# Kernel tuning notes

Hardware: AMD Instinct MI355X
Metric: run time of the kernel (lower is better)

The kernel has to match this reference:

```python
import jax, jax.numpy as jnp
import numpy as np

RADIUS = 0.2
NUM_POINTS = 32
MAX_POINTS = 60
BN_EPS = 1e-5


def _bn(x, g, b, m, v):
    # BatchNorm in eval mode (running stats), channels-last broadcast
    return g * (x - m) * jax.lax.rsqrt(v + BN_EPS) + b


def setup_inputs() -> dict:
    key = jax.random.key(0)
    nk = lambda i: jax.random.fold_in(key, i)
    B, NQ, NC, HC = 2, 4096, 8192, 64
    inp = {}
    inp['p_query'] = jax.random.uniform(nk(0), (B, NQ, 3), dtype=jnp.float32)
    inp['p_context'] = jax.random.uniform(nk(1), (B, NC, 3), dtype=jnp.float32)
    inp['h_context'] = jax.random.normal(nk(2), (B, NC, HC), dtype=jnp.float32)

    def lin(i, o, ci):
        return (jax.random.normal(nk(i), (o, ci), jnp.float32) / np.sqrt(ci).astype(np.float32),
                0.01 * jax.random.normal(nk(i + 1), (o,), jnp.float32))

    def bnp(i, c):
        return (1.0 + 0.1 * jax.random.normal(nk(i), (c,), jnp.float32),
                0.1 * jax.random.normal(nk(i + 1), (c,), jnp.float32),
                0.1 * jax.random.normal(nk(i + 2), (c,), jnp.float32),
                0.5 + jax.random.uniform(nk(i + 3), (c,), jnp.float32))

    inp['w_xyz'], inp['b_xyz'] = lin(10, 64, 3)
    # pointwise 1x1 Conv2d MLP: 128 -> 128 -> 128 -> 256 (BN after each conv)
    inp['pw_w1'], inp['pw_b1'] = lin(12, 128, 128)
    inp['pw_g1'], inp['pw_be1'], inp['pw_m1'], inp['pw_v1'] = bnp(14, 128)
    inp['pw_w2'], inp['pw_b2'] = lin(20, 128, 128)
    inp['pw_g2'], inp['pw_be2'], inp['pw_m2'], inp['pw_v2'] = bnp(22, 128)
    inp['pw_w3'], inp['pw_b3'] = lin(28, 256, 128)
    inp['pw_g3'], inp['pw_be3'], inp['pw_m3'], inp['pw_v3'] = bnp(30, 256)
    # global 1x1 Conv1d MLP: 256 -> 128 -> 64 -> 3 (BN+ReLU between, none on last)
    inp['g_w1'], inp['g_b1'] = lin(36, 128, 256)
    inp['g_g1'], inp['g_be1'], inp['g_m1'], inp['g_v1'] = bnp(38, 128)
    inp['g_w2'], inp['g_b2'] = lin(44, 64, 128)
    inp['g_g2'], inp['g_be2'], inp['g_m2'], inp['g_v2'] = bnp(46, 64)
    inp['g_w3'], inp['g_b3'] = lin(52, 3, 64)
    return inp


def reference(p_query, p_context, h_context, w_xyz, b_xyz,
              pw_w1, pw_b1, pw_g1, pw_be1, pw_m1, pw_v1,
              pw_w2, pw_b2, pw_g2, pw_be2, pw_m2, pw_v2,
              pw_w3, pw_b3, pw_g3, pw_be3, pw_m3, pw_v3,
              g_w1, g_b1, g_g1, g_be1, g_m1, g_v1,
              g_w2, g_b2, g_g2, g_be2, g_m2, g_v2,
              g_w3, g_b3):
    N = p_context.shape[1]
    # knn_points: squared distances, K smallest sorted ascending
    d = (jnp.sum(p_query ** 2, -1)[:, :, None]
         - 2.0 * jnp.einsum('bqd,bnd->bqn', p_query, p_context)
         + jnp.sum(p_context ** 2, -1)[:, None, :])  # [B,NQ,NC]
    neg, idx = jax.lax.top_k(-d, MAX_POINTS)
    dist = -neg  # [B,NQ,K] ascending
    knn_idx = jnp.where(dist > RADIUS ** 2, N + 1, idx)
    idx = knn_idx[:, :, :NUM_POINTS]
    dist = dist[:, :, :NUM_POINTS]
    mask = idx == N + 1
    idx = jnp.where(mask, 0, idx)
    dist = jnp.where(mask, 0.0, dist)
    gather = jax.vmap(lambda a, i: a[i])
    pts = gather(p_context, idx)        # [B,NQ,P,3]
    h_group = gather(h_context, idx)    # [B,NQ,P,HC]
    p_rel = pts - p_query[:, :, None, :]
    h_rel = p_rel @ w_xyz.T + b_xyz     # Linear(3 -> 64)
    h = jnp.concatenate([h_rel, h_group], -1)  # [B,NQ,P,128]
    h = jax.nn.relu(_bn(h @ pw_w1.T + pw_b1, pw_g1, pw_be1, pw_m1, pw_v1))
    h = jax.nn.relu(_bn(h @ pw_w2.T + pw_b2, pw_g2, pw_be2, pw_m2, pw_v2))
    h = _bn(h @ pw_w3.T + pw_b3, pw_g3, pw_be3, pw_m3, pw_v3)  # [B,NQ,P,256]
    # cosine radius weighting (note: dist is SQUARED distance, faithful to source)
    c = 0.5 * (jnp.cos(dist * (np.pi / RADIUS)) + 1.0)
    c = jnp.where((dist <= RADIUS) & (dist > 0.0), c, 0.0)
    y = jnp.sum(h * c[..., None], axis=2)  # masked weighted pool over neighbors -> [B,NQ,256]
    y = jax.nn.relu(_bn(y @ g_w1.T + g_b1, g_g1, g_be1, g_m1, g_v1))
    y = jax.nn.relu(_bn(y @ g_w2.T + g_b2, g_g2, g_be2, g_m2, g_v2))
    return y @ g_w3.T + g_b3  # [B,NQ,3]
```

## Files before the change

kernel.cpp:

```cpp
#include <hip/hip_runtime.h>
#include <hip/hip_bf16.h>
#include <math.h>

#define BB 2
#define NQ 4096
#define NC 8192
#define KNN 32
#define WCAP 512
#define QB 4
#define MROWS 128
#define BN_EPS 1e-5f

typedef __attribute__((ext_vector_type(8))) short s16x8;
typedef __attribute__((ext_vector_type(4))) float f32x4;

#define WS_IDX   0
#define WS_CW    1048576
#define WS_Z     2097152
#define WS_SQ    6291456
#define WS_PCF   6324224
#define WS_PIDX  6586368
#define WS_CELL  6651904
#define WS_CCNT  6717440
#define WS_COFS  6718464
#define WS_W1    6719488
#define WS_W2    6752256
#define WS_W3    6785024
#define WS_GW1   6850560
#define WS_GW2   6916096
#define WS_F3    6932480
#define WS_FG1   6934528
#define WS_FG2   6935552

__device__ inline int swz(int row, int kbyte, int rb) {
    return row * rb + (kbyte ^ ((row & 7) << 4));
}
__device__ inline unsigned short f2bf(float x) {
    __hip_bfloat16 h = __float2bfloat16(x);
    return *reinterpret_cast<unsigned short*>(&h);
}
__device__ inline float bf2f(unsigned short u) {
    return __uint_as_float(((unsigned)u) << 16);
}
__device__ inline int cell1d(float x) {
    int c = (int)floorf(x * 5.0f);
    return c < 0 ? 0 : (c > 4 ? 4 : c);
}

__device__ inline void mk_img(const float* __restrict__ src, int R, int K, char* dst, int t, int NT)
{
    int rbg = (K * 2) / 16;
    int ng = R * rbg;
    for (int g = t; g < ng; g += NT) {
        int row = g / rbg;
        int b16 = (g - row * rbg) * 16;
        int sb  = b16 ^ ((row & 7) << 4);
        const float* s = src + row * K + sb / 2;
        union { s16x8 v; unsigned short u[8]; } pk;
#pragma unroll
        for (int j = 0; j < 8; ++j) pk.u[j] = f2bf(s[j]);
        *(s16x8*)(dst + row * (K * 2) + b16) = pk.v;
    }
}

__global__ __launch_bounds__(256) void prep_kernel(
    const float* __restrict__ pc,
    const float* __restrict__ w1, const float* __restrict__ w2, const float* __restrict__ w3,
    const float* __restrict__ gw1, const float* __restrict__ gw2,
    const float* __restrict__ g3, const float* __restrict__ b3, const float* __restrict__ m3,
    const float* __restrict__ v3, const float* __restrict__ be3,
    const float* __restrict__ gg1, const float* __restrict__ gb1, const float* __restrict__ gm1,
    const float* __restrict__ gv1, const float* __restrict__ gbe1,
    const float* __restrict__ gg2, const float* __restrict__ gb2, const float* __restrict__ gm2,
    const float* __restrict__ gv2, const float* __restrict__ gbe2,
    char* __restrict__ ws)
{
    const int t = blockIdx.x * 256 + threadIdx.x;
    const int NT = gridDim.x * 256;

    int* cell = (int*)(ws + WS_CELL);
    int* ccnt = (int*)(ws + WS_CCNT);
    for (int i = t; i < BB * NC; i += NT) {
        float x = pc[i*3+0], y = pc[i*3+1], z = pc[i*3+2];
        int c = (cell1d(z)*5 + cell1d(y))*5 + cell1d(x);
        cell[i] = c;
        atomicAdd(&ccnt[(i >> 13)*128 + c], 1);
    }

    mk_img(w1,  128, 128, ws + WS_W1,  t, NT);
    mk_img(w2,  128, 128, ws + WS_W2,  t, NT);
    mk_img(w3,  256, 128, ws + WS_W3,  t, NT);
    mk_img(gw1, 128, 256, ws + WS_GW1, t, NT);
    mk_img(gw2,  64, 128, ws + WS_GW2, t, NT);

    if (t < 256) {
        float s = g3[t] * rsqrtf(v3[t] + BN_EPS);
        ((float2*)(ws + WS_F3))[t] = make_float2(s, s * (b3[t] - m3[t]) + be3[t]);
    }
    if (t < 128) {
        float s = gg1[t] * rsqrtf(gv1[t] + BN_EPS);
        ((float2*)(ws + WS_FG1))[t] = make_float2(s, s * (gb1[t] - gm1[t]) + gbe1[t]);
    }
    if (t < 64) {
        float s = gg2[t] * rsqrtf(gv2[t] + BN_EPS);
        ((float2*)(ws + WS_FG2))[t] = make_float2(s, s * (gb2[t] - gm2[t]) + gbe2[t]);
    }
}

__global__ __launch_bounds__(128) void scan_kernel(char* __restrict__ ws)
{
    int* ccnt = (int*)(ws + WS_CCNT);
    int* cofs = (int*)(ws + WS_COFS);
    const int wv = threadIdx.x >> 6, lane = threadIdx.x & 63;
    const int base = wv * 128;
    int a = (lane < 125) ? ccnt[base + lane] : 0;
    int b = (64 + lane < 125) ? ccnt[base + 64 + lane] : 0;
    int ai = a, bi = b;
    for (int d = 1; d < 64; d <<= 1) {
        int t = __shfl_up(ai, d, 64);
        if (lane >= d) ai += t;
    }
    int totA = __shfl(ai, 63, 64);
    for (int d = 1; d < 64; d <<= 1) {
        int t = __shfl_up(bi, d, 64);
        if (lane >= d) bi += t;
    }
    int exA = ai - a;
    int exB = totA + bi - b;
    cofs[base + lane] = exA;       cofs[base + 64 + lane] = exB;
    ccnt[base + lane] = exA;       ccnt[base + 64 + lane] = exB;
}

__global__ __launch_bounds__(256) void scatter_kernel(
    const float* __restrict__ pc, char* __restrict__ ws)
{
    const int i = blockIdx.x * 256 + threadIdx.x;
    if (i >= BB * NC) return;
    const int b = i >> 13, loc = i & (NC - 1);
    int* cell = (int*)(ws + WS_CELL);
    int* cur  = (int*)(ws + WS_CCNT);
    float4* pcf = (float4*)(ws + WS_PCF);
    int*    pidx = (int*)(ws + WS_PIDX);
    int c = cell[i];
    int pos = atomicAdd(&cur[b*128 + c], 1);
    float x = pc[i*3+0], y = pc[i*3+1], z = pc[i*3+2];
    float w = (x*x + y*y) + z*z;
    pcf[(size_t)b*NC + pos]  = make_float4(x, y, z, w);
    pidx[(size_t)b*NC + pos] = loc;
}

__device__ inline void cmpxu(unsigned long long& k, int j, bool up) {
    unsigned long long ok = __shfl_xor(k, j, 64);
    bool lower = ((threadIdx.x & 63) & j) == 0;
    bool take = (lower == up) ? (k > ok) : (k < ok);
    if (take) k = ok;
}
__device__ inline void sortasc64(unsigned long long& k) {
    const int lane = threadIdx.x & 63;
    for (int kk = 2; kk <= 64; kk <<= 1)
        for (int j = kk >> 1; j > 0; j >>= 1)
            cmpxu(k, j, (lane & kk) == 0);
}
__device__ inline void sortdesc64(unsigned long long& k) {
    const int lane = threadIdx.x & 63;
    for (int kk = 2; kk <= 64; kk <<= 1)
        for (int j = kk >> 1; j > 0; j >>= 1)
            cmpxu(k, j, (lane & kk) != 0);
}
__device__ inline void merge128(unsigned long long& k0, unsigned long long& k1) {
    if (k0 > k1) { unsigned long long t = k0; k0 = k1; k1 = t; }
#pragma unroll
    for (int j = 32; j > 0; j >>= 1) { cmpxu(k0, j, true); cmpxu(k1, j, true); }
}
__device__ inline void cmpx64(unsigned long long& k, int& p, int j, bool up) {
    unsigned long long ok = __shfl_xor(k, j, 64);
    int op = __shfl_xor(p, j, 64);
    bool lower = ((threadIdx.x & 63) & j) == 0;
    bool gt = (k > ok) || (k == ok && p > op);
    bool take = (lower == up) ? gt : !gt;
    if (take) { k = ok; p = op; }
}
__device__ inline void sortasc64kp(unsigned long long& k, int& p) {
    const int lane = threadIdx.x & 63;
    for (int kk = 2; kk <= 64; kk <<= 1)
        for (int j = kk >> 1; j > 0; j >>= 1)
            cmpx64(k, p, j, (lane & kk) == 0);
}

__global__ __launch_bounds__(256) void knn_kernel(
    const float* __restrict__ pq, const float* __restrict__ pc,
    const float4* __restrict__ pcf, const int* __restrict__ pidx,
    const int* __restrict__ cofs,
    int* __restrict__ idx_out, float* __restrict__ cw_out)
{
    __shared__ unsigned long long kbuf[4][WCAP];

    const int tid = threadIdx.x, lane = tid & 63, w = tid >> 6;
    const int gq = blockIdx.x * 4 + w;
    const int b = gq >> 12;

    const float qxf = pq[gq*3+0], qyf = pq[gq*3+1], qzf = pq[gq*3+2];
    const double qx = (double)qxf, qy = (double)qyf, qz = (double)qzf;
    const double sq = qx*qx + qy*qy + qz*qz;
    const float  sqf = (float)sq;
    const double R2d = 0.2 * 0.2;
    const float  R2f = 0.04f + 1e-4f;

    const float4* pcfb = pcf + (size_t)b * NC;
    const int*    pidb = pidx + (size_t)b * NC;
    const int*    cb   = cofs + b * 128;
    const float*  pcb  = pc + (size_t)b * NC * 3;

    int xlo = (int)floorf((qxf - 0.2f) * 5.0f - 1e-3f); xlo = xlo < 0 ? 0 : xlo;
    int xhi = (int)floorf((qxf + 0.2f) * 5.0f + 1e-3f); xhi = xhi > 4 ? 4 : xhi;
    int ylo = (int)floorf((qyf - 0.2f) * 5.0f - 1e-3f); ylo = ylo < 0 ? 0 : ylo;
    int yhi = (int)floorf((qyf + 0.2f) * 5.0f + 1e-3f); yhi = yhi > 4 ? 4 : yhi;
    int zlo = (int)floorf((qzf - 0.2f) * 5.0f - 1e-3f); zlo = zlo < 0 ? 0 : zlo;
    int zhi = (int)floorf((qzf + 0.2f) * 5.0f + 1e-3f); zhi = zhi > 4 ? 4 : zhi;

    const unsigned long long lt = (lane == 63) ? ~0ULL >> 1 : (1ULL << lane) - 1;
    int cnt = 0;
    for (int zi = zlo; zi <= zhi; ++zi) {
        for (int yi = ylo; yi <= yhi; ++yi) {
            int row = (zi*5 + yi)*5;
            int s = cb[row + xlo], e = cb[row + xhi + 1];
            for (int t0 = s; t0 < e; t0 += 64) {
                int t = t0 + lane;
                bool pred = false;
                unsigned long long key = ~0ULL;
                if (t < e) {
                    float4 cd = pcfb[t];
                    float dot = (qxf*cd.x + qyf*cd.y) + qzf*cd.z;
                    float d   = (sqf - 2.0f*dot) + cd.w;
                    pred = (d <= R2f);
                    if (pred) {
                        float dc = fmaxf(d, 0.0f);
                        key = ((unsigned long long)__float_as_uint(dc) << 32)
                            | (unsigned)pidb[t];
                    }
                }
                unsigned long long mask = __ballot(pred);
                if (pred) {
                    int pos = cnt + __popcll(mask & lt);
                    if (pos < WCAP) kbuf[w][pos] = key;
                }
                cnt += __popcll(mask);
            }
        }
    }
    if (cnt > WCAP) cnt = WCAP;

    unsigned long long k0 = (lane < cnt)      ? kbuf[w][lane]      : ~0ULL;
    unsigned long long k1 = (64 + lane < cnt) ? kbuf[w][64 + lane] : ~0ULL;
    sortasc64(k0);
    sortdesc64(k1);
    merge128(k0, k1);
    int consumed = 128;
    while (consumed < cnt) {
        int i1 = consumed + lane;
        k1 = (i1 < cnt) ? kbuf[w][i1] : ~0ULL;
        sortdesc64(k1);
        merge128(k0, k1);
        consumed += 64;
    }

    unsigned long long kf = ~0ULL;
    int pf = 0x7fffffff;
    if (k0 != ~0ULL) {
        int n = (int)(k0 & 0xffffffffULL);
        double cx = (double)pcb[n*3+0];
        double cy = (double)pcb[n*3+1];
        double cz = (double)pcb[n*3+2];
        double dot = qx*cx + qy*cy + qz*cz;
        double sc  = cx*cx + cy*cy + cz*cz;
        double d   = (sq - 2.0*dot) + sc;
        if (d <= R2d) {
            double dc = d < 0.0 ? 0.0 : d;
            kf = (unsigned long long)__double_as_longlong(dc);
            pf = n;
        }
    }
    sortasc64kp(kf, pf);

    if (lane < KNN) {
        int id = 0; float c = 0.0f;
        if (kf != ~0ULL) {
            id = pf;
            double d = __longlong_as_double((long long)kf);
            if (d > 0.0 && d <= 0.2) {
                double cw = 0.5 * (cos(d * 15.707963267948966) + 1.0);
                c = (float)cw;
            }
        }
        idx_out[gq*KNN + lane] = id;
        cw_out[gq*KNN + lane]  = c;
    }
}

__global__ __launch_bounds__(512, 4) void front_kernel(
    const float* __restrict__ pq, const float* __restrict__ pc, const float* __restrict__ hc,
    const float* __restrict__ w_xyz, const float* __restrict__ b_xyz,
    const float* __restrict__ b1, const float* __restrict__ g1,
    const float* __restrict__ be1, const float* __restrict__ m1, const float* __restrict__ v1,
    const float* __restrict__ b2, const float* __restrict__ g2,
    const float* __restrict__ be2, const float* __restrict__ m2, const float* __restrict__ v2,
    const char* __restrict__ w1img, const char* __restrict__ w2img,
    const int* __restrict__ idx_in, const float* __restrict__ cw_in,
    float* __restrict__ z_buf, float* __restrict__ sq_buf)
{
    __shared__ __align__(16) char smem[74240];
    char*  Ab   = smem;
    char*  Wb   = smem + 32768;
    float* Prel = (float*)(smem + 65536);
    float* Cw   = (float*)(smem + 67072);
    int*   Sidx = (int*)  (smem + 67584);
    float* Sfd  = (float*)(smem + 68096);
    float* Zp   = (float*)(smem + 70144);

    const int tid = threadIdx.x;
    const int qbase = blockIdx.x * QB;
    const int b = qbase >> 12;
    const float* pcb = pc + (size_t)b * NC * 3;
    const float* hcb = hc + (size_t)b * NC * 64;

    if (tid < MROWS) {
        int id = idx_in[qbase*KNN + tid];
        Sidx[tid] = id;
        Cw[tid]   = cw_in[qbase*KNN + tid];
        int gq = qbase + (tid >> 5);
        Prel[tid*3+0] = pcb[id*3+0] - pq[gq*3+0];
        Prel[tid*3+1] = pcb[id*3+1] - pq[gq*3+1];
        Prel[tid*3+2] = pcb[id*3+2] - pq[gq*3+2];
    }
    __syncthreads();

    for (int p = tid; p < MROWS*16; p += 512) {
        int row = p >> 4, seg = p & 15;
        float vals[8];
        if (seg >= 8) {
            const float* src = hcb + (size_t)Sidx[row]*64 + (seg-8)*8;
            float4 u0 = *(const float4*)src;
            float4 u1 = *(const float4*)(src+4);
            vals[0]=u0.x; vals[1]=u0.y; vals[2]=u0.z; vals[3]=u0.w;
            vals[4]=u1.x; vals[5]=u1.y; vals[6]=u1.z; vals[7]=u1.w;
        } else {
            float px = Prel[row*3+0], py = Prel[row*3+1], pz = Prel[row*3+2];
            int c0 = seg*8;
#pragma unroll
            for (int j = 0; j < 8; ++j) {
                int c = c0 + j;
                vals[j] = px*w_xyz[c*3+0] + py*w_xyz[c*3+1] + pz*w_xyz[c*3+2] + b_xyz[c];
            }
        }
        union { s16x8 v; unsigned short u[8]; } pk;
#pragma unroll
        for (int j = 0; j < 8; ++j) pk.u[j] = f2bf(vals[j]);
        *(s16x8*)(Ab + swz(row, seg*16, 256)) = pk.v;
    }
    if (tid < 128) {
        int j = tid;
        float s0 = g1[j] * rsqrtf(v1[j] + BN_EPS);
        Sfd[0*128 + j] = s0; Sfd[1*128 + j] = s0*(b1[j]-m1[j]) + be1[j];
        float s1 = g2[j] * rsqrtf(v2[j] + BN_EPS);
        Sfd[2*128 + j] = s1; Sfd[3*128 + j] = s1*(b2[j]-m2[j]) + be2[j];
    }
    if (tid < QB) {
        float s = 0.0f;
        for (int i = 0; i < KNN; ++i) s += Cw[tid*KNN + i];
        sq_buf[qbase + tid] = s;
    }

    const int l = tid & 63, w = tid >> 6;
    const int r0 = w * 16, cl = l & 15, q4 = l >> 4;

    {
        const s16x8* wimg = (const s16x8*)w1img;
        s16x8* Wv = (s16x8*)Wb;
        for (int p = tid; p < 2048; p += 512) Wv[p] = wimg[p];
        __syncthreads();

        f32x4 acc[8];
#pragma unroll
        for (int nt = 0; nt < 8; ++nt) acc[nt] = (f32x4){0.f,0.f,0.f,0.f};
#pragma unroll
        for (int kk = 0; kk < 4; ++kk) {
            int kbyte = kk*64 + q4*16;
            s16x8 a0 = *(const s16x8*)(Ab + swz(r0 + cl, kbyte, 256));
#pragma unroll
            for (int nt = 0; nt < 8; ++nt) {
                s16x8 bwv = *(const s16x8*)(Wb + swz(nt*16 + cl, kbyte, 256));
                acc[nt] = __builtin_amdgcn_mfma_f32_16x16x32_bf16(a0, bwv, acc[nt], 0, 0, 0);
            }
        }
#pragma unroll
        for (int nt = 0; nt < 8; ++nt) {
            int j = nt*16 + cl;
            float s = Sfd[0*128 + j], t = Sfd[1*128 + j];
#pragma unroll
            for (int r = 0; r < 4; ++r) {
                int row = r0 + q4*4 + r;
                float x = fmaxf(acc[nt][r]*s + t, 0.0f);
                unsigned int me = f2bf(x);
                unsigned int ot = (unsigned int)__shfl_xor((int)me, 1, 64);
                if ((cl & 1) == 0) {
                    unsigned int pk = me | (ot << 16);
                    *(unsigned int*)(Ab + swz(row, j*2, 256)) = pk;
                }
            }
        }
        __syncthreads();
    }

    {
        const s16x8* wimg = (const s16x8*)w2img;
        s16x8* Wv = (s16x8*)Wb;
        for (int p = tid; p < 2048; p += 512) Wv[p] = wimg[p];
        __syncthreads();

        f32x4 acc[8];
#pragma unroll
        for (int nt = 0; nt < 8; ++nt) acc[nt] = (f32x4){0.f,0.f,0.f,0.f};
#pragma unroll
        for (int kk = 0; kk < 4; ++kk) {
            int kbyte = kk*64 + q4*16;
            s16x8 a0 = *(const s16x8*)(Ab + swz(r0 + cl, kbyte, 256));
#pragma unroll
            for (int nt = 0; nt < 8; ++nt) {
                s16x8 bwv = *(const s16x8*)(Wb + swz(nt*16 + cl, kbyte, 256));
                acc[nt] = __builtin_amdgcn_mfma_f32_16x16x32_bf16(a0, bwv, acc[nt], 0, 0, 0);
            }
        }
        float cwr[4];
#pragma unroll
        for (int r = 0; r < 4; ++r) cwr[r] = Cw[r0 + q4*4 + r];
        float zp[8];
#pragma unroll
        for (int nt = 0; nt < 8; ++nt) {
            int j = nt*16 + cl;
            float s = Sfd[2*128 + j], t = Sfd[3*128 + j];
            float sum = 0.0f;
#pragma unroll
            for (int r = 0; r < 4; ++r) {
                float x = fmaxf(acc[nt][r]*s + t, 0.0f);
                sum += cwr[r] * x;
            }
            sum += __shfl_xor(sum, 16, 64);
            sum += __shfl_xor(sum, 32, 64);
            zp[nt] = sum;
        }
        if (q4 == 0) {
#pragma unroll
            for (int nt = 0; nt < 8; ++nt) Zp[w*128 + nt*16 + cl] = zp[nt];
        }
        __syncthreads();
    }

    {
        int q = tid >> 7, col = tid & 127;
        float z = Zp[(2*q)*128 + col] + Zp[(2*q+1)*128 + col];
        z_buf[(size_t)(qbase + q)*128 + col] = z;
    }
}

__global__ __launch_bounds__(256) void tail_kernel(
    const char* __restrict__ w3img, const char* __restrict__ gw1img, const char* __restrict__ gw2img,
    const float2* __restrict__ f3, const float2* __restrict__ fg1, const float2* __restrict__ fg2,
    const float* __restrict__ z_buf, const float* __restrict__ sq_buf,
    const float* __restrict__ gw3, const float* __restrict__ gb3,
    float* __restrict__ out)
{
    __shared__ __align__(16) char smem[123136];
    char* A1 = smem;
    char* A2 = smem + 16384;
    char* A4 = smem + 49152;
    char* Wb = smem + 57344;
    float* Ssm = (float*)(smem + 122880);

    const int tid = threadIdx.x;
    const int q0 = blockIdx.x * 64;

    for (int g = tid; g < 1024; g += 256) {
        int row = g >> 4, seg = g & 15;
        const float* zs = z_buf + (size_t)(q0 + row)*128 + seg*8;
        float4 u0 = *(const float4*)zs;
        float4 u1 = *(const float4*)(zs+4);
        union { s16x8 v; unsigned short u[8]; } pk;
        pk.u[0]=f2bf(u0.x); pk.u[1]=f2bf(u0.y); pk.u[2]=f2bf(u0.z); pk.u[3]=f2bf(u0.w);
        pk.u[4]=f2bf(u1.x); pk.u[5]=f2bf(u1.y); pk.u[6]=f2bf(u1.z); pk.u[7]=f2bf(u1.w);
        *(s16x8*)(A1 + swz(row, seg*16, 256)) = pk.v;
    }
    for (int p = tid; p < 4096; p += 256) ((s16x8*)Wb)[p] = ((const s16x8*)w3img)[p];
    if (tid < 64) Ssm[tid] = sq_buf[q0 + tid];
    __syncthreads();

    const int l = tid & 63, w = tid >> 6;
    const int r0 = w*16, cl = l & 15, q4 = l >> 4;

    {
        f32x4 acc[16];
#pragma unroll
        for (int nt = 0; nt < 16; ++nt) acc[nt] = (f32x4){0.f,0.f,0.f,0.f};
#pragma unroll
        for (int kk = 0; kk < 4; ++kk) {
            int kbyte = kk*64 + q4*16;
            s16x8 a0 = *(const s16x8*)(A1 + swz(r0 + cl, kbyte, 256));
#pragma unroll
            for (int nt = 0; nt < 16; ++nt) {
                s16x8 bwv = *(const s16x8*)(Wb + swz(nt*16 + cl, kbyte, 256));
                acc[nt] = __builtin_amdgcn_mfma_f32_16x16x32_bf16(a0, bwv, acc[nt], 0, 0, 0);
            }
        }
#pragma unroll
        for (int nt = 0; nt < 16; ++nt) {
            int j = nt*16 + cl;
            float2 f = f3[j];
#pragma unroll
            for (int r = 0; r < 4; ++r) {
                int row = r0 + q4*4 + r;
                float S = Ssm[row];
                float x = f.x*acc[nt][r] + S*f.y;
                *(unsigned short*)(A2 + swz(row, j*2, 512)) = f2bf(x);
            }
        }
    }
    __syncthreads();
    for (int p = tid; p < 4096; p += 256) ((s16x8*)Wb)[p] = ((const s16x8*)gw1img)[p];
    __syncthreads();

    {
        f32x4 acc[8];
#pragma unroll
        for (int nt = 0; nt < 8; ++nt) acc[nt] = (f32x4){0.f,0.f,0.f,0.f};
#pragma unroll
        for (int kk = 0; kk < 8; ++kk) {
            int kbyte = kk*64 + q4*16;
            s16x8 a0 = *(const s16x8*)(A2 + swz(r0 + cl, kbyte, 512));
#pragma unroll
            for (int nt = 0; nt < 8; ++nt) {
                s16x8 bwv = *(const s16x8*)(Wb + swz(nt*16 + cl, kbyte, 512));
                acc[nt] = __builtin_amdgcn_mfma_f32_16x16x32_bf16(a0, bwv, acc[nt], 0, 0, 0);
            }
        }
#pragma unroll
        for (int nt = 0; nt < 8; ++nt) {
            int j = nt*16 + cl;
            float2 f = fg1[j];
#pragma unroll
            for (int r = 0; r < 4; ++r) {
                int row = r0 + q4*4 + r;
                float x = fmaxf(f.x*acc[nt][r] + f.y, 0.0f);
                *(unsigned short*)(A1 + swz(row, j*2, 256)) = f2bf(x);
            }
        }
    }
    __syncthreads();
    for (int p = tid; p < 1024; p += 256) ((s16x8*)Wb)[p] = ((const s16x8*)gw2img)[p];
    __syncthreads();

    {
        f32x4 acc[4];
#pragma unroll
        for (int nt = 0; nt < 4; ++nt) acc[nt] = (f32x4){0.f,0.f,0.f,0.f};
#pragma unroll
        for (int kk = 0; kk < 4; ++kk) {
            int kbyte = kk*64 + q4*16;
            s16x8 a0 = *(const s16x8*)(A1 + swz(r0 + cl, kbyte, 256));
#pragma unroll
            for (int nt = 0; nt < 4; ++nt) {
                s16x8 bwv = *(const s16x8*)(Wb + swz(nt*16 + cl, kbyte, 256));
                acc[nt] = __builtin_amdgcn_mfma_f32_16x16x32_bf16(a0, bwv, acc[nt], 0, 0, 0);
            }
        }
#pragma unroll
        for (int nt = 0; nt < 4; ++nt) {
            int j = nt*16 + cl;
            float2 f = fg2[j];
#pragma unroll
            for (int r = 0; r < 4; ++r) {
                int row = r0 + q4*4 + r;
                float x = fmaxf(f.x*acc[nt][r] + f.y, 0.0f);
                *(unsigned short*)(A4 + swz(row, j*2, 128)) = f2bf(x);
            }
        }
    }
    __syncthreads();

    if (tid < 192) {
        int q = tid / 3, jj = tid - q*3;
        const float* wr = gw3 + jj*64;
        float s = 0.0f;
        for (int k = 0; k < 64; ++k) {
            unsigned short u = *(const unsigned short*)(A4 + swz(q, k*2, 128));
            s += bf2f(u) * wr[k];
        }
        out[(size_t)(q0 + q)*3 + jj] = s + gb3[jj];
    }
}

extern "C" void kernel_launch(void* const* d_in, const int* in_sizes, int n_in,
                              void* d_out, int out_size, void* d_ws, size_t ws_size,
                              hipStream_t stream)
{
    const float* pq    = (const float*)d_in[0];
    const float* pc    = (const float*)d_in[1];
    const float* hc    = (const float*)d_in[2];
    const float* w_xyz = (const float*)d_in[3];
    const float* b_xyz = (const float*)d_in[4];
    const float* w1    = (const float*)d_in[5];
    const float* b1    = (const float*)d_in[6];
    const float* g1    = (const float*)d_in[7];
    const float* be1   = (const float*)d_in[8];
    const float* m1    = (const float*)d_in[9];
    const float* v1    = (const float*)d_in[10];
    const float* w2    = (const float*)d_in[11];
    const float* b2    = (const float*)d_in[12];
    const float* g2    = (const float*)d_in[13];
    const float* be2   = (const float*)d_in[14];
    const float* m2    = (const float*)d_in[15];
    const float* v2    = (const float*)d_in[16];
    const float* w3    = (const float*)d_in[17];
    const float* b3    = (const float*)d_in[18];
    const float* g3    = (const float*)d_in[19];
    const float* be3   = (const float*)d_in[20];
    const float* m3    = (const float*)d_in[21];
    const float* v3    = (const float*)d_in[22];
    const float* gw1   = (const float*)d_in[23];
    const float* gb1   = (const float*)d_in[24];
    const float* gg1   = (const float*)d_in[25];
    const float* gbe1  = (const float*)d_in[26];
    const float* gm1   = (const float*)d_in[27];
    const float* gv1   = (const float*)d_in[28];
    const float* gw2   = (const float*)d_in[29];
    const float* gb2   = (const float*)d_in[30];
    const float* gg2   = (const float*)d_in[31];
    const float* gbe2  = (const float*)d_in[32];
    const float* gm2   = (const float*)d_in[33];
    const float* gv2   = (const float*)d_in[34];
    const float* gw3   = (const float*)d_in[35];
    const float* gb3   = (const float*)d_in[36];

    char* ws = (char*)d_ws;
    int*   idx_buf = (int*)(ws + WS_IDX);
    float* cw_buf  = (float*)(ws + WS_CW);
    float* z_buf   = (float*)(ws + WS_Z);
    float* sq_buf  = (float*)(ws + WS_SQ);

    hipMemsetAsync(ws + WS_CCNT, 0, 1024, stream);

    prep_kernel<<<64, 256, 0, stream>>>(pc, w1, w2, w3, gw1, gw2,
        g3, b3, m3, v3, be3, gg1, gb1, gm1, gv1, gbe1, gg2, gb2, gm2, gv2, gbe2, ws);

    scan_kernel<<<1, 128, 0, stream>>>(ws);

    scatter_kernel<<<(BB*NC + 255)/256, 256, 0, stream>>>(pc, ws);

    knn_kernel<<<(BB*NQ)/4, 256, 0, stream>>>(pq, pc,
        (const float4*)(ws + WS_PCF), (const int*)(ws + WS_PIDX),
        (const int*)(ws + WS_COFS), idx_buf, cw_buf);

    front_kernel<<<(BB*NQ)/QB, 512, 0, stream>>>(pq, pc, hc, w_xyz, b_xyz,
        b1, g1, be1, m1, v1, b2, g2, be2, m2, v2,
        ws + WS_W1, ws + WS_W2, idx_buf, cw_buf, z_buf, sq_buf);

    tail_kernel<<<(BB*NQ)/64, 256, 0, stream>>>(
        ws + WS_W3, ws + WS_GW1, ws + WS_GW2,
        (const float2*)(ws + WS_F3), (const float2*)(ws + WS_FG1), (const float2*)(ws + WS_FG2),
        z_buf, sq_buf, gw3, gb3, (float*)d_out);
}
```

Before: 149.8 us.

## Restructure front kernel to one query per wavefront without block barriers

The front kernel now assigns one query (32 neighbour rows) to each wavefront with a private LDS slice. All __syncthreads calls go away, and the shared weight staging is dropped, so the B operands are read directly from the global/L2 weight images. BN folding for the two pointwise layers moves into the prep kernel. The neighbour-weight sum becomes a wave shuffle reduction and z is written straight to global memory. This removes block-level barriers and the LDS weight copies, at the cost of repeated global reads of the weights for every wave.

New measurement: 165.1 us. 1.1x slower.

```diff
diff --git a/kernel.cpp b/kernel.cpp
--- a/kernel.cpp
+++ b/kernel.cpp
@@ -7,8 +7,6 @@
 #define NC 8192
 #define KNN 32
 #define WCAP 512
-#define QB 4
-#define MROWS 128
 #define BN_EPS 1e-5f
 
 typedef __attribute__((ext_vector_type(8))) short s16x8;
@@ -31,6 +29,8 @@
 #define WS_F3    6932480
 #define WS_FG1   6934528
 #define WS_FG2   6935552
+#define WS_FD1   6936064
+#define WS_FD2   6937088
 
 __device__ inline int swz(int row, int kbyte, int rb) {
     return row * rb + (kbyte ^ ((row & 7) << 4));
@@ -67,6 +67,10 @@
     const float* __restrict__ pc,
     const float* __restrict__ w1, const float* __restrict__ w2, const float* __restrict__ w3,
     const float* __restrict__ gw1, const float* __restrict__ gw2,
+    const float* __restrict__ b1, const float* __restrict__ g1, const float* __restrict__ m1,
+    const float* __restrict__ v1, const float* __restrict__ be1,
+    const float* __restrict__ b2, const float* __restrict__ g2, const float* __restrict__ m2,
+    const float* __restrict__ v2, const float* __restrict__ be2,
     const float* __restrict__ g3, const float* __restrict__ b3, const float* __restrict__ m3,
     const float* __restrict__ v3, const float* __restrict__ be3,
     const float* __restrict__ gg1, const float* __restrict__ gb1, const float* __restrict__ gm1,
@@ -100,6 +104,10 @@
     if (t < 128) {
         float s = gg1[t] * rsqrtf(gv1[t] + BN_EPS);
         ((float2*)(ws + WS_FG1))[t] = make_float2(s, s * (gb1[t] - gm1[t]) + gbe1[t]);
+        float s0 = g1[t] * rsqrtf(v1[t] + BN_EPS);
+        ((float2*)(ws + WS_FD1))[t] = make_float2(s0, s0 * (b1[t] - m1[t]) + be1[t]);
+        float s1 = g2[t] * rsqrtf(v2[t] + BN_EPS);
+        ((float2*)(ws + WS_FD2))[t] = make_float2(s1, s1 * (b2[t] - m2[t]) + be2[t]);
     }
     if (t < 64) {
         float s = gg2[t] * rsqrtf(gv2[t] + BN_EPS);
@@ -297,44 +305,49 @@
     }
 }
 
-__global__ __launch_bounds__(512, 4) void front_kernel(
+__global__ __launch_bounds__(256, 2) void front_kernel(
     const float* __restrict__ pq, const float* __restrict__ pc, const float* __restrict__ hc,
     const float* __restrict__ w_xyz, const float* __restrict__ b_xyz,
-    const float* __restrict__ b1, const float* __restrict__ g1,
-    const float* __restrict__ be1, const float* __restrict__ m1, const float* __restrict__ v1,
-    const float* __restrict__ b2, const float* __restrict__ g2,
-    const float* __restrict__ be2, const float* __restrict__ m2, const float* __restrict__ v2,
     const char* __restrict__ w1img, const char* __restrict__ w2img,
+    const float2* __restrict__ fd1, const float2* __restrict__ fd2,
     const int* __restrict__ idx_in, const float* __restrict__ cw_in,
     float* __restrict__ z_buf, float* __restrict__ sq_buf)
 {
-    __shared__ __align__(16) char smem[74240];
-    char*  Ab   = smem;
-    char*  Wb   = smem + 32768;
-    float* Prel = (float*)(smem + 65536);
-    float* Cw   = (float*)(smem + 67072);
-    int*   Sidx = (int*)  (smem + 67584);
-    float* Sfd  = (float*)(smem + 68096);
-    float* Zp   = (float*)(smem + 70144);
-
-    const int tid = threadIdx.x;
-    const int qbase = blockIdx.x * QB;
-    const int b = qbase >> 12;
+    __shared__ __align__(16) char smem[35840];
+    const int tid = threadIdx.x, lane = tid & 63, w = tid >> 6;
+    char*  slice = smem + w * 8960;
+    int*   Sidx  = (int*)  (slice + 8192);
+    float* Cwl   = (float*)(slice + 8320);
+    float* Prel  = (float*)(slice + 8448);
+
+    const int gq = blockIdx.x * 4 + w;
+    const int b = gq >> 12;
     const float* pcb = pc + (size_t)b * NC * 3;
     const float* hcb = hc + (size_t)b * NC * 64;
 
-    if (tid < MROWS) {
-        int id = idx_in[qbase*KNN + tid];
-        Sidx[tid] = id;
-        Cw[tid]   = cw_in[qbase*KNN + tid];
-        int gq = qbase + (tid >> 5);
-        Prel[tid*3+0] = pcb[id*3+0] - pq[gq*3+0];
-        Prel[tid*3+1] = pcb[id*3+1] - pq[gq*3+1];
-        Prel[tid*3+2] = pcb[id*3+2] - pq[gq*3+2];
-    }
-    __syncthreads();
-
-    for (int p = tid; p < MROWS*16; p += 512) {
+    float cwv = 0.0f;
+    if (lane < 32) {
+        int id = idx_in[gq*KNN + lane];
+        cwv = cw_in[gq*KNN + lane];
+        Sidx[lane] = id;
+        Cwl[lane]  = cwv;
+        Prel[lane*3+0] = pcb[id*3+0] - pq[gq*3+0];
+        Prel[lane*3+1] = pcb[id*3+1] - pq[gq*3+1];
+        Prel[lane*3+2] = pcb[id*3+2] - pq[gq*3+2];
+    }
+    {
+        float sv = cwv;
+        sv += __shfl_xor(sv, 1, 64);
+        sv += __shfl_xor(sv, 2, 64);
+        sv += __shfl_xor(sv, 4, 64);
+        sv += __shfl_xor(sv, 8, 64);
+        sv += __shfl_xor(sv, 16, 64);
+        if (lane == 0) sq_buf[gq] = sv;
+    }
+
+#pragma unroll 1
+    for (int it = 0; it < 8; ++it) {
+        int p = it*64 + lane;
         int row = p >> 4, seg = p & 15;
         float vals[8];
         if (seg >= 8) {
@@ -355,110 +368,87 @@
         union { s16x8 v; unsigned short u[8]; } pk;
 #pragma unroll
         for (int j = 0; j < 8; ++j) pk.u[j] = f2bf(vals[j]);
-        *(s16x8*)(Ab + swz(row, seg*16, 256)) = pk.v;
-    }
-    if (tid < 128) {
-        int j = tid;
-        float s0 = g1[j] * rsqrtf(v1[j] + BN_EPS);
-        Sfd[0*128 + j] = s0; Sfd[1*128 + j] = s0*(b1[j]-m1[j]) + be1[j];
-        float s1 = g2[j] * rsqrtf(v2[j] + BN_EPS);
-        Sfd[2*128 + j] = s1; Sfd[3*128 + j] = s1*(b2[j]-m2[j]) + be2[j];
-    }
-    if (tid < QB) {
-        float s = 0.0f;
-        for (int i = 0; i < KNN; ++i) s += Cw[tid*KNN + i];
-        sq_buf[qbase + tid] = s;
-    }
-
-    const int l = tid & 63, w = tid >> 6;
-    const int r0 = w * 16, cl = l & 15, q4 = l >> 4;
+        *(s16x8*)(slice + swz(row, seg*16, 256)) = pk.v;
+    }
+
+    const int cl = lane & 15, q4 = lane >> 4;
 
     {
-        const s16x8* wimg = (const s16x8*)w1img;
-        s16x8* Wv = (s16x8*)Wb;
-        for (int p = tid; p < 2048; p += 512) Wv[p] = wimg[p];
-        __syncthreads();
-
-        f32x4 acc[8];
-#pragma unroll
-        for (int nt = 0; nt < 8; ++nt) acc[nt] = (f32x4){0.f,0.f,0.f,0.f};
+        f32x4 acc[2][8];
+#pragma unroll
+        for (int m = 0; m < 2; ++m)
+#pragma unroll
+            for (int nt = 0; nt < 8; ++nt) acc[m][nt] = (f32x4){0.f,0.f,0.f,0.f};
 #pragma unroll
         for (int kk = 0; kk < 4; ++kk) {
             int kbyte = kk*64 + q4*16;
-            s16x8 a0 = *(const s16x8*)(Ab + swz(r0 + cl, kbyte, 256));
+            s16x8 a0 = *(const s16x8*)(slice + swz(cl,      kbyte, 256));
+            s16x8 a1 = *(const s16x8*)(slice + swz(16 + cl, kbyte, 256));
 #pragma unroll
             for (int nt = 0; nt < 8; ++nt) {
-                s16x8 bwv = *(const s16x8*)(Wb + swz(nt*16 + cl, kbyte, 256));
-                acc[nt] = __builtin_amdgcn_mfma_f32_16x16x32_bf16(a0, bwv, acc[nt], 0, 0, 0);
+                s16x8 bwv = *(const s16x8*)(w1img + swz(nt*16 + cl, kbyte, 256));
+                acc[0][nt] = __builtin_amdgcn_mfma_f32_16x16x32_bf16(a0, bwv, acc[0][nt], 0, 0, 0);
+                acc[1][nt] = __builtin_amdgcn_mfma_f32_16x16x32_bf16(a1, bwv, acc[1][nt], 0, 0, 0);
             }
         }
 #pragma unroll
         for (int nt = 0; nt < 8; ++nt) {
             int j = nt*16 + cl;
-            float s = Sfd[0*128 + j], t = Sfd[1*128 + j];
-#pragma unroll
-            for (int r = 0; r < 4; ++r) {
-                int row = r0 + q4*4 + r;
-                float x = fmaxf(acc[nt][r]*s + t, 0.0f);
-                unsigned int me = f2bf(x);
-                unsigned int ot = (unsigned int)__shfl_xor((int)me, 1, 64);
-                if ((cl & 1) == 0) {
-                    unsigned int pk = me | (ot << 16);
-                    *(unsigned int*)(Ab + swz(row, j*2, 256)) = pk;
+            float2 f = fd1[j];
+#pragma unroll
+            for (int m = 0; m < 2; ++m)
+#pragma unroll
+                for (int r = 0; r < 4; ++r) {
+                    int row = m*16 + q4*4 + r;
+                    float x = fmaxf(acc[m][nt][r]*f.x + f.y, 0.0f);
+                    unsigned int me = f2bf(x);
+                    unsigned int ot = (unsigned int)__shfl_xor((int)me, 1, 64);
+                    if ((cl & 1) == 0) {
+                        *(unsigned int*)(slice + swz(row, j*2, 256)) = me | (ot << 16);
+                    }
                 }
-            }
-        }
-        __syncthreads();
+        }
     }
 
     {
-        const s16x8* wimg = (const s16x8*)w2img;
-        s16x8* Wv = (s16x8*)Wb;
-        for (int p = tid; p < 2048; p += 512) Wv[p] = wimg[p];
-        __syncthreads();
-
-        f32x4 acc[8];
-#pragma unroll
-        for (int nt = 0; nt < 8; ++nt) acc[nt] = (f32x4){0.f,0.f,0.f,0.f};
+        f32x4 acc[2][8];
+#pragma unroll
+        for (int m = 0; m < 2; ++m)
+#pragma unroll
+            for (int nt = 0; nt < 8; ++nt) acc[m][nt] = (f32x4){0.f,0.f,0.f,0.f};
 #pragma unroll
         for (int kk = 0; kk < 4; ++kk) {
             int kbyte = kk*64 + q4*16;
-            s16x8 a0 = *(const s16x8*)(Ab + swz(r0 + cl, kbyte, 256));
+            s16x8 a0 = *(const s16x8*)(slice + swz(cl,      kbyte, 256));
+            s16x8 a1 = *(const s16x8*)(slice + swz(16 + cl, kbyte, 256));
 #pragma unroll
             for (int nt = 0; nt < 8; ++nt) {
-                s16x8 bwv = *(const s16x8*)(Wb + swz(nt*16 + cl, kbyte, 256));
-                acc[nt] = __builtin_amdgcn_mfma_f32_16x16x32_bf16(a0, bwv, acc[nt], 0, 0, 0);
-            }
-        }
-        float cwr[4];
-#pragma unroll
-        for (int r = 0; r < 4; ++r) cwr[r] = Cw[r0 + q4*4 + r];
-        float zp[8];
+                s16x8 bwv = *(const s16x8*)(w2img + swz(nt*16 + cl, kbyte, 256));
+                acc[0][nt] = __builtin_amdgcn_mfma_f32_16x16x32_bf16(a0, bwv, acc[0][nt], 0, 0, 0);
+                acc[1][nt] = __builtin_amdgcn_mfma_f32_16x16x32_bf16(a1, bwv, acc[1][nt], 0, 0, 0);
+            }
+        }
+        float cwr[2][4];
+#pragma unroll
+        for (int m = 0; m < 2; ++m)
+#pragma unroll
+            for (int r = 0; r < 4; ++r) cwr[m][r] = Cwl[m*16 + q4*4 + r];
 #pragma unroll
         for (int nt = 0; nt < 8; ++nt) {
             int j = nt*16 + cl;
-            float s = Sfd[2*128 + j], t = Sfd[3*128 + j];
+            float2 f = fd2[j];
             float sum = 0.0f;
 #pragma unroll
-            for (int r = 0; r < 4; ++r) {
-                float x = fmaxf(acc[nt][r]*s + t, 0.0f);
-                sum += cwr[r] * x;
-            }
+            for (int m = 0; m < 2; ++m)
+#pragma unroll
+                for (int r = 0; r < 4; ++r) {
+                    float x = fmaxf(acc[m][nt][r]*f.x + f.y, 0.0f);
+                    sum += cwr[m][r] * x;
+                }
             sum += __shfl_xor(sum, 16, 64);
             sum += __shfl_xor(sum, 32, 64);
-            zp[nt] = sum;
-        }
-        if (q4 == 0) {
-#pragma unroll
-            for (int nt = 0; nt < 8; ++nt) Zp[w*128 + nt*16 + cl] = zp[nt];
-        }
-        __syncthreads();
-    }
-
-    {
-        int q = tid >> 7, col = tid & 127;
-        float z = Zp[(2*q)*128 + col] + Zp[(2*q+1)*128 + col];
-        z_buf[(size_t)(qbase + q)*128 + col] = z;
+            if (q4 == 0) z_buf[(size_t)gq*128 + j] = sum;
+        }
     }
 }
 
@@ -648,6 +638,7 @@
     hipMemsetAsync(ws + WS_CCNT, 0, 1024, stream);
 
     prep_kernel<<<64, 256, 0, stream>>>(pc, w1, w2, w3, gw1, gw2,
+        b1, g1, m1, v1, be1, b2, g2, m2, v2, be2,
         g3, b3, m3, v3, be3, gg1, gb1, gm1, gv1, gbe1, gg2, gb2, gm2, gv2, gbe2, ws);
 
     scan_kernel<<<1, 128, 0, stream>>>(ws);
@@ -658,9 +649,10 @@
         (const float4*)(ws + WS_PCF), (const int*)(ws + WS_PIDX),
         (const int*)(ws + WS_COFS), idx_buf, cw_buf);
 
-    front_kernel<<<(BB*NQ)/QB, 512, 0, stream>>>(pq, pc, hc, w_xyz, b_xyz,
-        b1, g1, be1, m1, v1, b2, g2, be2, m2, v2,
-        ws + WS_W1, ws + WS_W2, idx_buf, cw_buf, z_buf, sq_buf);
+    front_kernel<<<(BB*NQ)/4, 256, 0, stream>>>(pq, pc, hc, w_xyz, b_xyz,
+        ws + WS_W1, ws + WS_W2,
+        (const float2*)(ws + WS_FD1), (const float2*)(ws + WS_FD2),
+        idx_buf, cw_buf, z_buf, sq_buf);
 
     tail_kernel<<<(BB*NQ)/64, 256, 0, stream>>>(
         ws + WS_W3, ws + WS_GW1, ws + WS_GW2,
```
